# Optimization experiments

Hardware: AMD Instinct MI355X
Metric: run time of the kernel (lower is better)

The kernel has to match this reference:

```python
import jax, jax.numpy as jnp
import numpy as np

B = 512
EPS = 1e-5


def _coords():
    # cvt_coord(i) = [(i//5 - 2)/2, (i%5 - 2)/2] on a 5x5 grid
    c = np.array([[(i // 5 - 2) / 2.0, (i % 5 - 2) / 2.0] for i in range(25)], dtype=np.float32)
    return jnp.asarray(c)  # [25, 2]


def setup_inputs() -> dict:
    key = jax.random.key(0)
    ks = jax.random.split(key, 32)
    d = {
        'img': jax.random.normal(ks[0], (B, 3, 75, 75), jnp.float32),
        'qst': jax.random.normal(ks[1], (B, 11), jnp.float32),
    }
    # conv backbone params
    cin = [3, 24, 24, 24]
    for l in range(4):
        d[f'conv_w{l+1}'] = jax.random.normal(ks[2 + l], (24, cin[l], 3, 3), jnp.float32) * 0.1
        d[f'conv_b{l+1}'] = jnp.zeros((24,), jnp.float32)
        d[f'bn_g{l+1}'] = 1.0 + 0.05 * jax.random.normal(ks[6 + l], (24,), jnp.float32)
        d[f'bn_b{l+1}'] = 0.05 * jax.random.normal(ks[10 + l], (24,), jnp.float32)
    # g MLP (63->256, 256->256 x3)
    d['g_w1'] = jax.random.normal(ks[14], (256, 63), jnp.float32) * 0.05
    d['g_b1'] = jnp.zeros((256,), jnp.float32)
    for l in (2, 3, 4):
        d[f'g_w{l}'] = jax.random.normal(ks[13 + l], (256, 256), jnp.float32) * 0.05
        d[f'g_b{l}'] = jnp.zeros((256,), jnp.float32)
    # f MLP and output head
    d['f_w1'] = jax.random.normal(ks[20], (256, 256), jnp.float32) * 0.05
    d['f_b1'] = jnp.zeros((256,), jnp.float32)
    d['fc2_w'] = jax.random.normal(ks[21], (256, 256), jnp.float32) * 0.05
    d['fc2_b'] = jnp.zeros((256,), jnp.float32)
    d['fc3_w'] = jax.random.normal(ks[22], (10, 256), jnp.float32) * 0.05
    d['fc3_b'] = jnp.zeros((10,), jnp.float32)
    return d


def _conv_bn(x, w, b, g, be):
    y = jax.lax.conv_general_dilated(x, w, (2, 2), [(1, 1), (1, 1)],
                                     dimension_numbers=('NCHW', 'OIHW', 'NCHW'))
    y = jax.nn.relu(y + b[None, :, None, None])
    # BatchNorm2d with batch statistics (training-mode forward)
    mu = jnp.mean(y, axis=(0, 2, 3), keepdims=True)
    var = jnp.var(y, axis=(0, 2, 3), keepdims=True)
    return (y - mu) * jax.lax.rsqrt(var + EPS) * g[None, :, None, None] + be[None, :, None, None]


def _lin(x, w, b):
    return x @ w.T + b


def reference(img, qst,
              conv_w1, conv_b1, bn_g1, bn_b1,
              conv_w2, conv_b2, bn_g2, bn_b2,
              conv_w3, conv_b3, bn_g3, bn_b3,
              conv_w4, conv_b4, bn_g4, bn_b4,
              g_w1, g_b1, g_w2, g_b2, g_w3, g_b3, g_w4, g_b4,
              f_w1, f_b1, fc2_w, fc2_b, fc3_w, fc3_b):
    x = _conv_bn(img, conv_w1, conv_b1, bn_g1, bn_b1)
    x = _conv_bn(x, conv_w2, conv_b2, bn_g2, bn_b2)
    x = _conv_bn(x, conv_w3, conv_b3, bn_g3, bn_b3)
    x = _conv_bn(x, conv_w4, conv_b4, bn_g4, bn_b4)  # [B, 24, 5, 5]
    mb = x.shape[0]
    x_flat = x.reshape(mb, 24, 25).transpose(0, 2, 1)  # [B, 25, 24]
    coords = jnp.broadcast_to(_coords()[None], (mb, 25, 2))
    x_flat = jnp.concatenate([x_flat, coords], axis=2)  # [B, 25, 26]
    # all-pairs: pair (p, q) -> concat(obj_q, obj_p, qst)
    xj = jnp.concatenate([x_flat, jnp.broadcast_to(qst[:, None, :], (mb, 25, 11))], axis=2)  # [B,25,37]
    x_i = jnp.broadcast_to(x_flat[:, None, :, :], (mb, 25, 25, 26))
    x_j = jnp.broadcast_to(xj[:, :, None, :], (mb, 25, 25, 37))
    x_full = jnp.concatenate([x_i, x_j], axis=3).reshape(mb * 625, 63)
    h = jax.nn.relu(_lin(x_full, g_w1, g_b1))
    h = jax.nn.relu(_lin(h, g_w2, g_b2))
    h = jax.nn.relu(_lin(h, g_w3, g_b3))
    h = jax.nn.relu(_lin(h, g_w4, g_b4))
    x_g = h.reshape(mb, 625, 256).sum(axis=1)  # [B, 256]
    x_f = jax.nn.relu(_lin(x_g, f_w1, f_b1))
    x_f = jax.nn.relu(_lin(x_f, fc2_w, fc2_b))  # (dropout omitted: eval/deterministic)
    logits = _lin(x_f, fc3_w, fc3_b)
    return jax.nn.log_softmax(logits, axis=-1)
```

## Files before the change

### kernel.cpp

```cpp
#include <hip/hip_runtime.h>
#include <hip/hip_bf16.h>

#define EPS 1e-5f

typedef _Float16 half_t;
typedef __attribute__((ext_vector_type(8))) _Float16 h16x8;
typedef __attribute__((ext_vector_type(4))) _Float16 h16x4;
typedef __attribute__((ext_vector_type(4))) float f32x4;

__device__ __forceinline__ float relu_f(float x) { return x > 0.f ? x : 0.f; }

#define OFF_Y1   0
#define OFF_Y2   17743872
#define OFF_Y3   22179840
#define OFF_Y4   23408640
#define OFF_ST   23715840
#define OFF_WHL  23718912
#define OFF_A    0
#define OFF_BV   3276800
#define OFF_XG   6553600

__global__ __launch_bounds__(256) void k_prep(const float* w2, const float* w3,
                                              const float* w4, half_t* whl, float* stats) {
    int idx = blockIdx.x * 256 + threadIdx.x;
    if (idx < 3072) stats[idx] = 0.f;
    int l = idx >> 16, e = idx & 65535;
    const float* w = (l == 0) ? w2 : (l == 1) ? w3 : w4;
    float v = w[e];
    int c = e >> 8, k = e & 255;
    int o = ((c >> 4) * 8 + (k >> 5)) * 512 + ((k >> 3) & 3) * 128 + (c & 15) * 8 + (k & 7);
    whl[l * 65536 + o] = (half_t)v;
}

__global__ __launch_bounds__(256, 2) void k_conv1(const float* img, const float* w,
                                                  const float* bias, half_t* y1, float* ostats) {
    __shared__ float wl[648], bl[24], red[4][48];
    int tid = threadIdx.x;
    if (tid < 24) bl[tid] = bias[tid];
    for (int i = tid; i < 648; i += 256) wl[i] = w[i];
    __syncthreads();
    int idx = blockIdx.x * 256 + tid;
    int b2 = idx / 1444, rem = idx % 1444;
    int b0 = b2 * 2;
    int oh = rem / 38, ow = rem % 38;
    float acc0[24], acc1[24];
#pragma unroll
    for (int o = 0; o < 24; ++o) { acc0[o] = bl[o]; acc1[o] = bl[o]; }
    for (int ic = 0; ic < 3; ++ic) {
        float p0[9], p1[9];
#pragma unroll
        for (int kh = 0; kh < 3; ++kh) {
            int ih = oh * 2 - 1 + kh;
#pragma unroll
            for (int kw = 0; kw < 3; ++kw) {
                int iw = ow * 2 - 1 + kw;
                bool ok = (unsigned)ih < 75u && (unsigned)iw < 75u;
                p0[kh * 3 + kw] = ok ? img[((b0 * 3 + ic) * 75 + ih) * 75 + iw] : 0.f;
                p1[kh * 3 + kw] = ok ? img[(((b0 + 1) * 3 + ic) * 75 + ih) * 75 + iw] : 0.f;
            }
        }
#pragma unroll
        for (int o = 0; o < 24; ++o)
#pragma unroll
            for (int t = 0; t < 9; ++t) {
                float wv = wl[(o * 3 + ic) * 9 + t];
                acc0[o] += wv * p0[t];
                acc1[o] += wv * p1[t];
            }
    }
    int wave = tid >> 6;
#pragma unroll
    for (int o = 0; o < 24; ++o) {
        acc0[o] = relu_f(acc0[o]);
        acc1[o] = relu_f(acc1[o]);
        y1[(b0 * 24 + o) * 1444 + rem] = (half_t)acc0[o];
        y1[((b0 + 1) * 24 + o) * 1444 + rem] = (half_t)acc1[o];
        float v = acc0[o] + acc1[o];
        float v2 = acc0[o] * acc0[o] + acc1[o] * acc1[o];
#pragma unroll
        for (int off = 1; off < 64; off <<= 1) { v += __shfl_xor(v, off); v2 += __shfl_xor(v2, off); }
        if ((tid & 63) == 0) { red[wave][o] = v; red[wave][24 + o] = v2; }
    }
    __syncthreads();
    if (tid < 48)
        atomicAdd(&ostats[(blockIdx.x & 15) * 48 + tid],
                  red[0][tid] + red[1][tid] + red[2][tid] + red[3][tid]);
}

__global__ __launch_bounds__(256, 2) void k_conv2(const half_t* yin, const float* w,
                                                  const float* bias, const float* instats,
                                                  const float* bng, const float* bnb,
                                                  float* yout, float* ostats) {
    __shared__ float wl[5184], bl[24], sc[24], sh[24], red[4][48];
    int tid = threadIdx.x;
    if (tid < 24) {
        float s = 0.f, s2 = 0.f;
#pragma unroll
        for (int k = 0; k < 16; ++k) { s += instats[k * 48 + tid]; s2 += instats[k * 48 + 24 + tid]; }
        float mu = s * (1.f / 739328.f);
        float var = s2 * (1.f / 739328.f) - mu * mu;
        float sca = bng[tid] * rsqrtf(var + EPS);
        sc[tid] = sca; sh[tid] = bnb[tid] - mu * sca;
        bl[tid] = bias[tid];
    }
    for (int i = tid; i < 5184; i += 256) wl[i] = w[i];
    __syncthreads();
    int idx = blockIdx.x * 256 + tid;
    int b2 = idx / 361, rem = idx % 361;
    int b0 = b2 * 2;
    int oh = rem / 19, ow = rem % 19;
    float acc0[24], acc1[24];
#pragma unroll
    for (int o = 0; o < 24; ++o) { acc0[o] = bl[o]; acc1[o] = bl[o]; }
    for (int ic = 0; ic < 24; ++ic) {
        float p0[9], p1[9];
        float scc = sc[ic], shc = sh[ic];
#pragma unroll
        for (int kh = 0; kh < 3; ++kh) {
            int ih = oh * 2 - 1 + kh;
#pragma unroll
            for (int kw = 0; kw < 3; ++kw) {
                int iw = ow * 2 - 1 + kw;
                bool ok = (unsigned)ih < 38u && (unsigned)iw < 38u;
                p0[kh * 3 + kw] = ok ? (float)yin[((b0 * 24 + ic) * 38 + ih) * 38 + iw] * scc + shc : 0.f;
                p1[kh * 3 + kw] = ok ? (float)yin[(((b0 + 1) * 24 + ic) * 38 + ih) * 38 + iw] * scc + shc : 0.f;
            }
        }
#pragma unroll
        for (int o = 0; o < 24; ++o)
#pragma unroll
            for (int t = 0; t < 9; ++t) {
                float wv = wl[(o * 24 + ic) * 9 + t];
                acc0[o] += wv * p0[t];
                acc1[o] += wv * p1[t];
            }
    }
    int wave = tid >> 6;
#pragma unroll
    for (int o = 0; o < 24; ++o) {
        acc0[o] = relu_f(acc0[o]);
        acc1[o] = relu_f(acc1[o]);
        yout[(b0 * 24 + o) * 361 + rem] = acc0[o];
        yout[((b0 + 1) * 24 + o) * 361 + rem] = acc1[o];
        float v = acc0[o] + acc1[o];
        float v2 = acc0[o] * acc0[o] + acc1[o] * acc1[o];
#pragma unroll
        for (int off = 1; off < 64; off <<= 1) { v += __shfl_xor(v, off); v2 += __shfl_xor(v2, off); }
        if ((tid & 63) == 0) { red[wave][o] = v; red[wave][24 + o] = v2; }
    }
    __syncthreads();
    if (tid < 48)
        atomicAdd(&ostats[(blockIdx.x & 15) * 48 + tid],
                  red[0][tid] + red[1][tid] + red[2][tid] + red[3][tid]);
}

__global__ __launch_bounds__(256) void k_conv(const float* yin, const float* w,
                                              const float* bias, const float* instats,
                                              const float* bng, const float* bnb,
                                              float* yout, float* ostats,
                                              int Hin, int Hout, float invN) {
    __shared__ float wl[5184], bl[24], sc[24], sh[24], red[4][48];
    int tid = threadIdx.x;
    if (tid < 24) {
        float s = 0.f, s2 = 0.f;
#pragma unroll
        for (int k = 0; k < 16; ++k) { s += instats[k * 48 + tid]; s2 += instats[k * 48 + 24 + tid]; }
        float mu = s * invN;
        float var = s2 * invN - mu * mu;
        float sca = bng[tid] * rsqrtf(var + EPS);
        sc[tid] = sca; sh[tid] = bnb[tid] - mu * sca;
        bl[tid] = bias[tid];
    }
    for (int i = tid; i < 5184; i += 256) wl[i] = w[i];
    __syncthreads();
    int idx = blockIdx.x * 256 + tid;
    int HWo = Hout * Hout;
    int b = idx / HWo, rem = idx % HWo;
    int oh = rem / Hout, ow = rem % Hout;
    float acc[24];
#pragma unroll
    for (int o = 0; o < 24; ++o) acc[o] = bl[o];
    for (int ic = 0; ic < 24; ++ic) {
        float patch[9];
        float scc = sc[ic], shc = sh[ic];
#pragma unroll
        for (int kh = 0; kh < 3; ++kh) {
            int ih = oh * 2 - 1 + kh;
#pragma unroll
            for (int kw = 0; kw < 3; ++kw) {
                int iw = ow * 2 - 1 + kw;
                bool ok = (unsigned)ih < (unsigned)Hin && (unsigned)iw < (unsigned)Hin;
                patch[kh * 3 + kw] = ok ? yin[((b * 24 + ic) * Hin + ih) * Hin + iw] * scc + shc : 0.f;
            }
        }
#pragma unroll
        for (int o = 0; o < 24; ++o)
#pragma unroll
            for (int t = 0; t < 9; ++t) acc[o] += wl[(o * 24 + ic) * 9 + t] * patch[t];
    }
    int wave = tid >> 6;
#pragma unroll
    for (int o = 0; o < 24; ++o) {
        acc[o] = relu_f(acc[o]);
        yout[(b * 24 + o) * HWo + rem] = acc[o];
        float v = acc[o], v2 = v * v;
#pragma unroll
        for (int off = 1; off < 64; off <<= 1) { v += __shfl_xor(v, off); v2 += __shfl_xor(v2, off); }
        if ((tid & 63) == 0) { red[wave][o] = v; red[wave][24 + o] = v2; }
    }
    __syncthreads();
    if (tid < 48)
        atomicAdd(&ostats[(blockIdx.x & 15) * 48 + tid],
                  red[0][tid] + red[1][tid] + red[2][tid] + red[3][tid]);
}

__global__ __launch_bounds__(256) void k_obj(const float* y4, const float* qst,
                                             const float* w1, const float* b1,
                                             const float* instats, const float* bng,
                                             const float* bnb, float* A, float* Bv, float* xg) {
    int b = blockIdx.x, tid = threadIdx.x;
    __shared__ float w1l[16128];
    __shared__ float objs[25][28];
    __shared__ float sc[24], sh[24], q[11];
    xg[b * 256 + tid] = 0.f;
    for (int i = tid; i < 16128; i += 256) w1l[i] = w1[i];
    if (tid < 24) {
        float s = 0.f, s2 = 0.f;
#pragma unroll
        for (int k = 0; k < 16; ++k) { s += instats[k * 48 + tid]; s2 += instats[k * 48 + 24 + tid]; }
        float mu = s * (1.f / 12800.f);
        float var = s2 * (1.f / 12800.f) - mu * mu;
        float sca = bng[tid] * rsqrtf(var + EPS);
        sc[tid] = sca; sh[tid] = bnb[tid] - mu * sca;
    }
    if (tid < 11) q[tid] = qst[b * 11 + tid];
    __syncthreads();
    for (int i = tid; i < 600; i += 256) {
        int c = i / 25, p = i % 25;
        objs[p][c] = y4[b * 600 + i] * sc[c] + sh[c];
    }
    if (tid < 25) { objs[tid][24] = ((tid / 5) - 2) * 0.5f; objs[tid][25] = ((tid % 5) - 2) * 0.5f; }
    __syncthreads();
    float wr[63];
#pragma unroll
    for (int k = 0; k < 63; ++k) wr[k] = w1l[tid * 63 + k];
    float qdot = b1[tid];
#pragma unroll
    for (int j = 0; j < 11; ++j) qdot += wr[52 + j] * q[j];
#pragma unroll 1
    for (int p = 0; p < 25; ++p) {
        float a = 0.f, bv = qdot;
#pragma unroll
        for (int k = 0; k < 26; ++k) { a += wr[k] * objs[p][k]; bv += wr[26 + k] * objs[p][k]; }
        A[(b * 25 + p) * 256 + tid] = a;
        Bv[(b * 25 + p) * 256 + tid] = bv;
    }
}

__global__ __launch_bounds__(256, 4) void k_g(const float* A, const float* Bv, const half_t* whl,
                                              const float* gb2, const float* gb3,
                                              const float* gb4, float* xg) {
    __shared__ alignas(16) half_t h[64 * 264];
    __shared__ float biasL[3][256];
    int tid = threadIdx.x;
    int lb = (blockIdx.x & 7) * 640 + (blockIdx.x >> 3);
    int b = lb / 10, t = lb % 10;
    int r0 = t * 64;
    int rmax = 625 - r0; if (rmax > 64) rmax = 64;
    biasL[0][tid] = gb2[tid];
    biasL[1][tid] = gb3[tid];
    biasL[2][tid] = gb4[tid];
    const float* Ab = A + b * 6400;
    const float* Bb = Bv + b * 6400;
#pragma unroll
    for (int it = 0; it < 16; ++it) {
        int r = it * 4 + (tid >> 6);
        int rs = __builtin_amdgcn_readfirstlane(r);
        int pr = r0 + rs; if (pr > 624) pr = 624;
        int i = pr % 25, j = pr / 25;
        int c4 = (tid & 63) << 2;
        float4 av = *(const float4*)&Ab[i * 256 + c4];
        float4 bv = *(const float4*)&Bb[j * 256 + c4];
        h16x4 hv = {(half_t)relu_f(av.x + bv.x), (half_t)relu_f(av.y + bv.y),
                    (half_t)relu_f(av.z + bv.z), (half_t)relu_f(av.w + bv.w)};
        *(h16x4*)&h[r * 264 + c4] = hv;
    }
    __syncthreads();
    int cg = tid >> 6, lane = tid & 63;
    int quad = lane >> 4, l15 = lane & 15;
    const half_t* hr = h + l15 * 264;
    const half_t* Wl = whl + (cg * 4) * 8 * 512 + lane * 8;
#pragma unroll 1
    for (int layer = 0; layer < 3; ++layer) {
        const half_t* W = Wl + layer * 65536;
        f32x4 acc[4][4];
#pragma unroll
        for (int mi = 0; mi < 4; ++mi)
#pragma unroll
            for (int nt = 0; nt < 4; ++nt) acc[mi][nt] = (f32x4){0.f, 0.f, 0.f, 0.f};
        h16x8 aw0 = *(const h16x8*)&W[0 * 4096];
        h16x8 aw1 = *(const h16x8*)&W[1 * 4096];
        h16x8 aw2 = *(const h16x8*)&W[2 * 4096];
        h16x8 aw3 = *(const h16x8*)&W[3 * 4096];
        h16x8 bh0 = *(const h16x8*)&hr[0 * 4224 + quad * 8];
        h16x8 bh1 = *(const h16x8*)&hr[1 * 4224 + quad * 8];
#pragma unroll 2
        for (int ks = 0; ks < 8; ++ks) {
            int ko = ks * 32 + quad * 8;
            int ksn = (ks + 1) & 7;
            int kon = ksn * 32 + quad * 8;
            h16x8 bh2 = *(const h16x8*)&hr[2 * 4224 + ko];
            h16x8 bh3 = *(const h16x8*)&hr[3 * 4224 + ko];
            h16x8 an0 = *(const h16x8*)&W[0 * 4096 + ksn * 512];
            h16x8 an1 = *(const h16x8*)&W[1 * 4096 + ksn * 512];
            h16x8 an2 = *(const h16x8*)&W[2 * 4096 + ksn * 512];
            h16x8 an3 = *(const h16x8*)&W[3 * 4096 + ksn * 512];
            __builtin_amdgcn_s_setprio(1);
            acc[0][0] = __builtin_amdgcn_mfma_f32_16x16x32_f16(aw0, bh0, acc[0][0], 0, 0, 0);
            acc[1][0] = __builtin_amdgcn_mfma_f32_16x16x32_f16(aw1, bh0, acc[1][0], 0, 0, 0);
            acc[2][0] = __builtin_amdgcn_mfma_f32_16x16x32_f16(aw2, bh0, acc[2][0], 0, 0, 0);
            acc[3][0] = __builtin_amdgcn_mfma_f32_16x16x32_f16(aw3, bh0, acc[3][0], 0, 0, 0);
            acc[0][1] = __builtin_amdgcn_mfma_f32_16x16x32_f16(aw0, bh1, acc[0][1], 0, 0, 0);
            acc[1][1] = __builtin_amdgcn_mfma_f32_16x16x32_f16(aw1, bh1, acc[1][1], 0, 0, 0);
            acc[2][1] = __builtin_amdgcn_mfma_f32_16x16x32_f16(aw2, bh1, acc[2][1], 0, 0, 0);
            acc[3][1] = __builtin_amdgcn_mfma_f32_16x16x32_f16(aw3, bh1, acc[3][1], 0, 0, 0);
            h16x8 bn0 = *(const h16x8*)&hr[0 * 4224 + kon];
            h16x8 bn1 = *(const h16x8*)&hr[1 * 4224 + kon];
            acc[0][2] = __builtin_amdgcn_mfma_f32_16x16x32_f16(aw0, bh2, acc[0][2], 0, 0, 0);
            acc[1][2] = __builtin_amdgcn_mfma_f32_16x16x32_f16(aw1, bh2, acc[1][2], 0, 0, 0);
            acc[2][2] = __builtin_amdgcn_mfma_f32_16x16x32_f16(aw2, bh2, acc[2][2], 0, 0, 0);
            acc[3][2] = __builtin_amdgcn_mfma_f32_16x16x32_f16(aw3, bh2, acc[3][2], 0, 0, 0);
            acc[0][3] = __builtin_amdgcn_mfma_f32_16x16x32_f16(aw0, bh3, acc[0][3], 0, 0, 0);
            acc[1][3] = __builtin_amdgcn_mfma_f32_16x16x32_f16(aw1, bh3, acc[1][3], 0, 0, 0);
            acc[2][3] = __builtin_amdgcn_mfma_f32_16x16x32_f16(aw2, bh3, acc[2][3], 0, 0, 0);
            acc[3][3] = __builtin_amdgcn_mfma_f32_16x16x32_f16(aw3, bh3, acc[3][3], 0, 0, 0);
            __builtin_amdgcn_s_setprio(0);
            aw0 = an0; aw1 = an1; aw2 = an2; aw3 = an3;
            bh0 = bn0; bh1 = bn1;
        }
        __syncthreads();
        if (layer < 2) {
#pragma unroll
            for (int mi = 0; mi < 4; ++mi) {
                int c0 = cg * 64 + mi * 16 + quad * 4;
#pragma unroll
                for (int nt = 0; nt < 4; ++nt) {
                    int row = nt * 16 + l15;
                    h16x4 hv;
#pragma unroll
                    for (int v = 0; v < 4; ++v)
                        hv[v] = (half_t)relu_f(acc[mi][nt][v] + biasL[layer][c0 + v]);
                    *(h16x4*)&h[row * 264 + c0] = hv;
                }
            }
            __syncthreads();
        } else {
#pragma unroll
            for (int mi = 0; mi < 4; ++mi) {
                int c0 = cg * 64 + mi * 16 + quad * 4;
#pragma unroll
                for (int v = 0; v < 4; ++v) {
                    float s = 0.f;
#pragma unroll
                    for (int nt = 0; nt < 4; ++nt) {
                        int row = nt * 16 + l15;
                        float x = relu_f(acc[mi][nt][v] + biasL[2][c0 + v]);
                        if (row < rmax) s += x;
                    }
                    s += __shfl_xor(s, 1);
                    s += __shfl_xor(s, 2);
                    s += __shfl_xor(s, 4);
                    s += __shfl_xor(s, 8);
                    if (l15 == 0) atomicAdd(&xg[b * 256 + c0 + v], s);
                }
            }
        }
    }
}

__global__ __launch_bounds__(256) void k_f(const float* xg, const float* fw1, const float* fb1,
                                           const float* fw2, const float* fb2,
                                           const float* fw3, const float* fb3, float* out) {
    int b0 = blockIdx.x * 2, tid = threadIdx.x;
    __shared__ float xb[2][256], h1[2][256], l10[2][10], red[2];
    xb[0][tid] = xg[b0 * 256 + tid];
    xb[1][tid] = xg[(b0 + 1) * 256 + tid];
    __syncthreads();
    float s0 = fb1[tid], s1 = s0;
    {
        const float4* wr = (const float4*)&fw1[tid * 256];
        const float4* x0 = (const float4*)xb[0];
        const float4* x1 = (const float4*)xb[1];
#pragma unroll 8
        for (int k = 0; k < 64; ++k) {
            float4 w = wr[k], a = x0[k], c = x1[k];
            s0 += w.x * a.x + w.y * a.y + w.z * a.z + w.w * a.w;
            s1 += w.x * c.x + w.y * c.y + w.z * c.z + w.w * c.w;
        }
    }
    h1[0][tid] = relu_f(s0);
    h1[1][tid] = relu_f(s1);
    __syncthreads();
    s0 = fb2[tid]; s1 = s0;
    {
        const float4* wr = (const float4*)&fw2[tid * 256];
        const float4* x0 = (const float4*)h1[0];
        const float4* x1 = (const float4*)h1[1];
#pragma unroll 8
        for (int k = 0; k < 64; ++k) {
            float4 w = wr[k], a = x0[k], c = x1[k];
            s0 += w.x * a.x + w.y * a.y + w.z * a.z + w.w * a.w;
            s1 += w.x * c.x + w.y * c.y + w.z * c.z + w.w * c.w;
        }
    }
    __syncthreads();
    xb[0][tid] = relu_f(s0);
    xb[1][tid] = relu_f(s1);
    __syncthreads();
    if (tid < 20) {
        int bb = tid / 10, o = tid % 10;
        float v = fb3[o];
        const float4* wr = (const float4*)&fw3[o * 256];
        const float4* hv = (const float4*)xb[bb];
#pragma unroll 8
        for (int k = 0; k < 64; ++k) {
            float4 w = wr[k], x = hv[k];
            v += w.x * x.x + w.y * x.y + w.z * x.z + w.w * x.w;
        }
        l10[bb][o] = v;
    }
    __syncthreads();
    if (tid < 2) {
        float m = l10[tid][0];
        for (int i = 1; i < 10; ++i) m = fmaxf(m, l10[tid][i]);
        float e = 0.f;
        for (int i = 0; i < 10; ++i) e += expf(l10[tid][i] - m);
        red[tid] = m + logf(e);
    }
    __syncthreads();
    if (tid < 20) {
        int bb = tid / 10, o = tid % 10;
        out[(b0 + bb) * 10 + o] = l10[bb][o] - red[bb];
    }
}

extern "C" void kernel_launch(void* const* d_in, const int* in_sizes, int n_in,
                              void* d_out, int out_size, void* d_ws, size_t ws_size,
                              hipStream_t stream) {
    const float* img = (const float*)d_in[0];
    const float* qst = (const float*)d_in[1];
    const float* cw[4] = {(const float*)d_in[2], (const float*)d_in[6],
                          (const float*)d_in[10], (const float*)d_in[14]};
    const float* cb[4] = {(const float*)d_in[3], (const float*)d_in[7],
                          (const float*)d_in[11], (const float*)d_in[15]};
    const float* bg[4] = {(const float*)d_in[4], (const float*)d_in[8],
                          (const float*)d_in[12], (const float*)d_in[16]};
    const float* bb[4] = {(const float*)d_in[5], (const float*)d_in[9],
                          (const float*)d_in[13], (const float*)d_in[17]};
    const float* gw1 = (const float*)d_in[18];
    const float* gb1 = (const float*)d_in[19];
    const float* gw2 = (const float*)d_in[20];
    const float* gb2 = (const float*)d_in[21];
    const float* gw3 = (const float*)d_in[22];
    const float* gb3 = (const float*)d_in[23];
    const float* gw4 = (const float*)d_in[24];
    const float* gb4 = (const float*)d_in[25];
    const float* fw1 = (const float*)d_in[26];
    const float* fb1 = (const float*)d_in[27];
    const float* fw2 = (const float*)d_in[28];
    const float* fb2 = (const float*)d_in[29];
    const float* fw3 = (const float*)d_in[30];
    const float* fb3 = (const float*)d_in[31];

    float* ws = (float*)d_ws;
    half_t* y1 = (half_t*)(ws + OFF_Y1);
    float* y2 = ws + OFF_Y2;
    float* y3 = ws + OFF_Y3;
    float* y4 = ws + OFF_Y4;
    float* st = ws + OFF_ST;
    half_t* whl = (half_t*)(ws + OFF_WHL);
    float* A = ws + OFF_A;
    float* Bv = ws + OFF_BV;
    float* xg = ws + OFF_XG;
    float* out = (float*)d_out;

    k_prep<<<768, 256, 0, stream>>>(gw2, gw3, gw4, whl, st);
    k_conv1<<<1444, 256, 0, stream>>>(img, cw[0], cb[0], y1, st + 0 * 768);
    k_conv2<<<361, 256, 0, stream>>>(y1, cw[1], cb[1], st + 0 * 768, bg[0], bb[0], y2,
                                     st + 1 * 768);
    k_conv<<<200, 256, 0, stream>>>(y2, cw[2], cb[2], st + 1 * 768, bg[1], bb[1], y3,
                                    st + 2 * 768, 19, 10, 1.f / 184832.f);
    k_conv<<<50, 256, 0, stream>>>(y3, cw[3], cb[3], st + 2 * 768, bg[2], bb[2], y4,
                                   st + 3 * 768, 10, 5, 1.f / 51200.f);
    k_obj<<<512, 256, 0, stream>>>(y4, qst, gw1, gb1, st + 3 * 768, bg[3], bb[3], A, Bv, xg);
    k_g<<<5120, 256, 0, stream>>>(A, Bv, whl, gb2, gb3, gb4, xg);
    k_f<<<256, 256, 0, stream>>>(xg, fw1, fb1, fw2, fb2, fw3, fb3, out);
}
```

Before: 623.0 us.

## Store conv1 output channels-last and vectorize conv2 input and weight loads

The conv1 intermediate now uses a pixel-major, channel-innermost fp16 layout and is written with 16-byte vector stores. Conv2 reads each input pixel's 24 channels with three vector loads and takes weights from a transposed shared layout as float4. BN scale and shift are kept in registers. The aim is to replace scattered 2-byte global accesses and scalar LDS reads with wide coalesced ones, at the cost of higher register pressure in conv2.

After: 2.155 ms. +246.0%, slower.

```diff
diff --git a/kernel.cpp b/kernel.cpp
--- a/kernel.cpp
+++ b/kernel.cpp
@@ -68,13 +68,19 @@
                 acc1[o] += wv * p1[t];
             }
     }
+#pragma unroll
+    for (int o = 0; o < 24; ++o) { acc0[o] = relu_f(acc0[o]); acc1[o] = relu_f(acc1[o]); }
+#pragma unroll
+    for (int g = 0; g < 3; ++g) {
+        h16x8 a, c;
+#pragma unroll
+        for (int j = 0; j < 8; ++j) { a[j] = (half_t)acc0[g * 8 + j]; c[j] = (half_t)acc1[g * 8 + j]; }
+        *(h16x8*)&y1[((long)(b0) * 1444 + rem) * 24 + g * 8] = a;
+        *(h16x8*)&y1[((long)(b0 + 1) * 1444 + rem) * 24 + g * 8] = c;
+    }
     int wave = tid >> 6;
 #pragma unroll
     for (int o = 0; o < 24; ++o) {
-        acc0[o] = relu_f(acc0[o]);
-        acc1[o] = relu_f(acc1[o]);
-        y1[(b0 * 24 + o) * 1444 + rem] = (half_t)acc0[o];
-        y1[((b0 + 1) * 24 + o) * 1444 + rem] = (half_t)acc1[o];
         float v = acc0[o] + acc1[o];
         float v2 = acc0[o] * acc0[o] + acc1[o] * acc1[o];
 #pragma unroll
@@ -91,7 +97,7 @@
                                                   const float* bias, const float* instats,
                                                   const float* bng, const float* bnb,
                                                   float* yout, float* ostats) {
-    __shared__ float wl[5184], bl[24], sc[24], sh[24], red[4][48];
+    __shared__ float wl[5184], bl[24], scs[24], shs[24], red[4][48];
     int tid = threadIdx.x;
     if (tid < 24) {
         float s = 0.f, s2 = 0.f;
@@ -100,11 +106,18 @@
         float mu = s * (1.f / 739328.f);
         float var = s2 * (1.f / 739328.f) - mu * mu;
         float sca = bng[tid] * rsqrtf(var + EPS);
-        sc[tid] = sca; sh[tid] = bnb[tid] - mu * sca;
+        scs[tid] = sca; shs[tid] = bnb[tid] - mu * sca;
         bl[tid] = bias[tid];
     }
-    for (int i = tid; i < 5184; i += 256) wl[i] = w[i];
-    __syncthreads();
+    for (int i = tid; i < 5184; i += 256) {
+        int t = i / 576, r = i % 576;
+        int o = r / 24, ic = r % 24;
+        wl[i] = w[(o * 24 + ic) * 9 + t];
+    }
+    __syncthreads();
+    float scr[24], shr[24];
+#pragma unroll
+    for (int ic = 0; ic < 24; ++ic) { scr[ic] = scs[ic]; shr[ic] = shs[ic]; }
     int idx = blockIdx.x * 256 + tid;
     int b2 = idx / 361, rem = idx % 361;
     int b0 = b2 * 2;
@@ -112,28 +125,45 @@
     float acc0[24], acc1[24];
 #pragma unroll
     for (int o = 0; o < 24; ++o) { acc0[o] = bl[o]; acc1[o] = bl[o]; }
-    for (int ic = 0; ic < 24; ++ic) {
-        float p0[9], p1[9];
-        float scc = sc[ic], shc = sh[ic];
-#pragma unroll
-        for (int kh = 0; kh < 3; ++kh) {
-            int ih = oh * 2 - 1 + kh;
-#pragma unroll
-            for (int kw = 0; kw < 3; ++kw) {
-                int iw = ow * 2 - 1 + kw;
-                bool ok = (unsigned)ih < 38u && (unsigned)iw < 38u;
-                p0[kh * 3 + kw] = ok ? (float)yin[((b0 * 24 + ic) * 38 + ih) * 38 + iw] * scc + shc : 0.f;
-                p1[kh * 3 + kw] = ok ? (float)yin[(((b0 + 1) * 24 + ic) * 38 + ih) * 38 + iw] * scc + shc : 0.f;
-            }
-        }
-#pragma unroll
-        for (int o = 0; o < 24; ++o)
-#pragma unroll
-            for (int t = 0; t < 9; ++t) {
-                float wv = wl[(o * 24 + ic) * 9 + t];
-                acc0[o] += wv * p0[t];
-                acc1[o] += wv * p1[t];
-            }
+#pragma unroll
+    for (int kh = 0; kh < 3; ++kh) {
+        int ih = oh * 2 - 1 + kh;
+#pragma unroll
+        for (int kw = 0; kw < 3; ++kw) {
+            int iw = ow * 2 - 1 + kw;
+            bool ok = (unsigned)ih < 38u && (unsigned)iw < 38u;
+            float p0[24], p1[24];
+            if (ok) {
+                long px = (long)ih * 38 + iw;
+                const half_t* s0 = &yin[((long)b0 * 1444 + px) * 24];
+                const half_t* s1 = &yin[((long)(b0 + 1) * 1444 + px) * 24];
+                h16x8 v00 = *(const h16x8*)&s0[0], v01 = *(const h16x8*)&s0[8], v02 = *(const h16x8*)&s0[16];
+                h16x8 v10 = *(const h16x8*)&s1[0], v11 = *(const h16x8*)&s1[8], v12 = *(const h16x8*)&s1[16];
+#pragma unroll
+                for (int j = 0; j < 8; ++j) {
+                    p0[j]      = (float)v00[j] * scr[j]      + shr[j];
+                    p0[8 + j]  = (float)v01[j] * scr[8 + j]  + shr[8 + j];
+                    p0[16 + j] = (float)v02[j] * scr[16 + j] + shr[16 + j];
+                    p1[j]      = (float)v10[j] * scr[j]      + shr[j];
+                    p1[8 + j]  = (float)v11[j] * scr[8 + j]  + shr[8 + j];
+                    p1[16 + j] = (float)v12[j] * scr[16 + j] + shr[16 + j];
+                }
+            } else {
+#pragma unroll
+                for (int ic = 0; ic < 24; ++ic) { p0[ic] = 0.f; p1[ic] = 0.f; }
+            }
+            const float* wt = &wl[(kh * 3 + kw) * 576];
+#pragma unroll
+            for (int o = 0; o < 24; ++o) {
+                const float4* w4 = (const float4*)&wt[o * 24];
+#pragma unroll
+                for (int q = 0; q < 6; ++q) {
+                    float4 wv = w4[q];
+                    acc0[o] += wv.x * p0[q * 4] + wv.y * p0[q * 4 + 1] + wv.z * p0[q * 4 + 2] + wv.w * p0[q * 4 + 3];
+                    acc1[o] += wv.x * p1[q * 4] + wv.y * p1[q * 4 + 1] + wv.z * p1[q * 4 + 2] + wv.w * p1[q * 4 + 3];
+                }
+            }
+        }
     }
     int wave = tid >> 6;
 #pragma unroll
```
